# Kernel optimization log

Measured on AMD Instinct MI355X. Metric: run time of the kernel, lower is better.

The kernel has to match this reference:

```python
import jax, jax.numpy as jnp
import numpy as np
from jax import lax

FEAT = 256      # feat_channels
GROUPS = 32     # GN num_groups
NCLS = 80       # num_classes - 1
NRAYS = 36      # polar mask rays
STACK = 4       # stacked_convs
SIZES = [(160, 256), (80, 128), (40, 64), (20, 32), (10, 16)]
B = 1


def conv(x, w, b=None):
    # 3x3 conv, stride 1, pad 1 (SAME). x: [N,C,H,W], w: [O,I,3,3]
    y = lax.conv_general_dilated(x, w, (1, 1), 'SAME',
                                 dimension_numbers=('NCHW', 'OIHW', 'NCHW'))
    if b is not None:
        y = y + b[None, :, None, None]
    return y


def group_norm(x, g, b, eps=1e-5):
    N, C, H, W = x.shape
    xr = x.reshape(N, GROUPS, C // GROUPS, H, W)
    m = xr.mean(axis=(2, 3, 4), keepdims=True)
    v = xr.var(axis=(2, 3, 4), keepdims=True)
    xr = (xr - m) * jax.lax.rsqrt(v + eps)
    return xr.reshape(N, C, H, W) * g[None, :, None, None] + b[None, :, None, None]


def tower(x, ws, gs, bs):
    # ConvModule: conv (no bias, norm present) -> GN -> ReLU, repeated STACK times
    for i in range(STACK):
        x = jax.nn.relu(group_norm(conv(x, ws[i]), gs[i], bs[i]))
    return x


def setup_inputs() -> dict:
    key = jax.random.key(0)
    ks = jax.random.split(key, 32)
    d = {}
    for l, (h, w) in enumerate(SIZES):
        d[f'feat{l}'] = jax.random.normal(ks[l], (B, FEAT, h, w), dtype=jnp.float32)
    std = 0.01
    for j, name in enumerate(['cls', 'reg', 'msk']):
        d[f'{name}_w'] = jax.random.normal(ks[5 + j], (STACK, FEAT, FEAT, 3, 3), jnp.float32) * std
        d[f'{name}_g'] = jnp.ones((STACK, FEAT), jnp.float32)
        d[f'{name}_b'] = jnp.zeros((STACK, FEAT), jnp.float32)
    bias_cls = float(-np.log((1 - 0.01) / 0.01))  # bias_init_with_prob(0.01)
    d['pcls_w'] = jax.random.normal(ks[10], (NCLS, FEAT, 3, 3), jnp.float32) * std
    d['pcls_b'] = jnp.full((NCLS,), bias_cls, jnp.float32)
    d['preg_w'] = jax.random.normal(ks[11], (4, FEAT, 3, 3), jnp.float32) * std
    d['preg_b'] = jnp.zeros((4,), jnp.float32)
    d['pmsk_w'] = jax.random.normal(ks[12], (NRAYS, FEAT, 3, 3), jnp.float32) * std
    d['pmsk_b'] = jnp.zeros((NRAYS,), jnp.float32)
    d['pctr_w'] = jax.random.normal(ks[13], (1, FEAT, 3, 3), jnp.float32) * std
    d['pctr_b'] = jnp.zeros((1,), jnp.float32)
    d['scales_bbox'] = jnp.ones((5,), jnp.float32)
    d['scales_mask'] = jnp.ones((5,), jnp.float32)
    return d


def reference(feat0, feat1, feat2, feat3, feat4,
              cls_w, cls_g, cls_b, reg_w, reg_g, reg_b, msk_w, msk_g, msk_b,
              pcls_w, pcls_b, preg_w, preg_b, pmsk_w, pmsk_b, pctr_w, pctr_b,
              scales_bbox, scales_mask):
    feats = [feat0, feat1, feat2, feat3, feat4]
    cls_outs, bbox_outs, ctr_outs, mask_outs = [], [], [], []
    for l, x in enumerate(feats):
        cf = tower(x, cls_w, cls_g, cls_b)
        cls_outs.append(conv(cf, pcls_w, pcls_b))
        ctr_outs.append(conv(cf, pctr_w, pctr_b))
        rf = tower(x, reg_w, reg_g, reg_b)
        bbox_outs.append(jnp.exp(conv(rf, preg_w, preg_b) * scales_bbox[l]))
        mf = tower(x, msk_w, msk_g, msk_b)
        mask_outs.append(jnp.exp(conv(mf, pmsk_w, pmsk_b) * scales_mask[l]))
    # multi_apply grouping: (cls_scores, bbox_preds, centernesses, mask_preds)
    return tuple(cls_outs) + tuple(bbox_outs) + tuple(ctr_outs) + tuple(mask_outs)
```

## Files before the change

### kernel.cpp

```cpp
#include <hip/hip_runtime.h>

typedef unsigned short u16;
typedef unsigned int u32;
typedef short bf16x8 __attribute__((ext_vector_type(8)));
typedef float f32x4 __attribute__((ext_vector_type(4)));

__device__ __forceinline__ float bf2f(u16 u) {
  u32 x = ((u32)u) << 16;
  float f;
  __builtin_memcpy(&f, &x, 4);
  return f;
}
__device__ __forceinline__ u16 f2bf(float f) {
  u32 x;
  __builtin_memcpy(&x, &f, 4);
  u32 r = x + 0x7FFFu + ((x >> 16) & 1u);
  return (u16)(r >> 16);
}
__device__ __forceinline__ u32 pack2(float f0, float f1) {
  u32 a, b;
  __builtin_memcpy(&a, &f0, 4);
  __builtin_memcpy(&b, &f1, 4);
  a += 0x8000u;
  b += 0x8000u;
  return __builtin_amdgcn_perm(b, a, 0x07060302);
}
__device__ __forceinline__ void glds16(const u16* g, u16* l) {
  __builtin_amdgcn_global_load_lds((const __attribute__((address_space(1))) u32*)g,
                                   (__attribute__((address_space(3))) u32*)l, 16, 0, 0);
}


__global__ void convert_weights(const float* __restrict__ cw, const float* __restrict__ rw,
                                const float* __restrict__ mw, const float* __restrict__ pc,
                                const float* __restrict__ pr, const float* __restrict__ pm,
                                const float* __restrict__ pt, u16* __restrict__ dst) {
  int e = blockIdx.x * 256 + threadIdx.x;
  if (e >= 7446528) return;
  float v = 0.f;
  if (e < 7077888) {
    int conv = e / 589824, r = e % 589824;
    int mo = r / 294912;
    int r2 = r - mo * 294912;
    int kt = r2 >> 12;
    int r3 = r2 & 4095;
    int wm = r3 >> 11;
    int mi = (r3 >> 9) & 3;
    int l = (r3 >> 3) & 63;
    int j = r3 & 7;
    int ch = kt / 9, ti = kt - ch * 9;
    int dxs = ti / 3, dys = ti - dxs * 3;
    int tap = dys * 3 + dxs;
    int o = mo * 128 + wm * 64 + mi * 16 + (l & 15);
    int c = ch * 32 + (l >> 4) * 8 + j;
    const float* s = (conv < 4) ? cw : (conv < 8) ? rw : mw;
    int si = conv & 3;
    v = s[((si * 256 + o) * 256 + c) * 9 + tap];
  } else {
    int e2 = e - 7077888;
    if (e2 < 221184) {
      int chunk = e2 / 27648, r = e2 % 27648;
      int tap = r / 3072, r2 = r % 3072;
      int g = r2 / 768;
      int o = (r2 - g * 768) >> 3;
      int c = chunk * 32 + g * 8 + (r2 & 7);
      if (o < 80) v = pc[(o * 256 + c) * 9 + tap];
      else if (o == 80) v = pt[c * 9 + tap];
    } else if (e2 < 258048) {
      int e3 = e2 - 221184;
      int chunk = e3 / 4608, r = e3 % 4608;
      int tap = r / 512, r2 = r % 512;
      int g = r2 >> 7;
      int o = (r2 >> 3) & 15;
      int c = chunk * 32 + g * 8 + (r2 & 7);
      if (o < 4) v = pr[(o * 256 + c) * 9 + tap];
    } else {
      int e3 = e2 - 258048;
      int chunk = e3 / 13824, r = e3 % 13824;
      int tap = r / 1536, r2 = r % 1536;
      int g = r2 / 384;
      int o = (r2 - g * 384) >> 3;
      int c = chunk * 32 + g * 8 + (r2 & 7);
      if (o < 36) v = pm[(o * 256 + c) * 9 + tap];
    }
  }
  dst[e] = f2bf(v);
}

__global__ void halo_zero(u16* __restrict__ X, u16* __restrict__ Y, long ACT, int ntw) {
  int i = blockIdx.x * 256 + threadIdx.x;
  int rep = i / 26112;
  int j = i - rep * 26112;
  if (rep >= 2 * ntw) return;
  int hp = j >> 4, sub = j & 15;
  int Wp, Hp, pxb, h;
  if (hp < 836)       { Wp = 258; Hp = 162; pxb = 0;     h = hp; }
  else if (hp < 1256) { Wp = 130; Hp = 82;  pxb = 41796; h = hp - 836; }
  else if (hp < 1468) { Wp = 66;  Hp = 42;  pxb = 52456; h = hp - 1256; }
  else if (hp < 1576) { Wp = 34;  Hp = 22;  pxb = 55228; h = hp - 1468; }
  else                { Wp = 18;  Hp = 12;  pxb = 55976; h = hp - 1576; }
  int y, x;
  if (h < Wp)          { y = 0;      x = h; }
  else if (h < 2 * Wp) { y = Hp - 1; x = h - Wp; }
  else {
    int rr = h - 2 * Wp;
    y = 1 + (rr >> 1);
    x = (rr & 1) ? (Wp - 1) : 0;
  }
  u16* buf = (rep < ntw) ? (X + rep * ACT) : (Y + (rep - ntw) * ACT);
  long adr = (long)(pxb + y * Wp + x) * 256 + sub * 16;
  uint4 z = {0, 0, 0, 0};
  *(uint4*)(buf + adr) = z;
  *(uint4*)(buf + adr + 8) = z;
}

__global__ void feat_to_nhwc(const float* __restrict__ f0, const float* __restrict__ f1,
                             const float* __restrict__ f2, const float* __restrict__ f3,
                             const float* __restrict__ f4, u16* __restrict__ dst,
                             long tstride, int nrep) {
  __shared__ float lds[64 * 65];
  int bx = blockIdx.x;
  int tile = bx >> 2, c0 = (bx & 3) * 64;
  int tl, sh, pxb, npx;
  const float* src;
  if (tile < 640)      { tl = tile;       sh = 8; pxb = 0;     npx = 40960; src = f0; }
  else if (tile < 800) { tl = tile - 640; sh = 7; pxb = 41796; npx = 10240; src = f1; }
  else if (tile < 840) { tl = tile - 800; sh = 6; pxb = 52456; npx = 2560;  src = f2; }
  else if (tile < 850) { tl = tile - 840; sh = 5; pxb = 55228; npx = 640;   src = f3; }
  else                 { tl = tile - 850; sh = 4; pxb = 55976; npx = 160;   src = f4; }
  int W = 1 << sh, Wp = W + 2;
  int px0 = tl * 64;
  int t = threadIdx.x;
  {
    int cc = (t >> 6) * 16, px = t & 63;
    bool ok = (px0 + px) < npx;
#pragma unroll
    for (int j = 0; j < 16; ++j) {
      float v = ok ? src[(c0 + cc + j) * npx + px0 + px] : 0.f;
      lds[(cc + j) * 65 + px] = v;
    }
  }
  __syncthreads();
  {
    int px = t >> 2, cL = (t & 3) * 16;
    int pxi = px0 + px;
    if (pxi < npx) {
      int y = pxi >> sh, x = pxi & (W - 1);
      u32 w[8];
#pragma unroll
      for (int j = 0; j < 8; ++j)
        w[j] = pack2(lds[(cL + 2 * j) * 65 + px], lds[(cL + 2 * j + 1) * 65 + px]);
      long adr = (long)(pxb + (y + 1) * Wp + (x + 1)) * 256 + c0 + cL;
      uint4 v0 = {w[0], w[1], w[2], w[3]}, v1 = {w[4], w[5], w[6], w[7]};
      for (int r = 0; r < nrep; ++r) {
        *(uint4*)(dst + r * tstride + adr) = v0;
        *(uint4*)(dst + r * tstride + adr + 8) = v1;
      }
    }
  }
}

__global__ void finalize_stats(const float* __restrict__ stats, int st_ts,
                               const float* __restrict__ g0, const float* __restrict__ g1,
                               const float* __restrict__ g2, const float* __restrict__ b0,
                               const float* __restrict__ b1, const float* __restrict__ b2,
                               float* __restrict__ scaleb, int sb_ts, int ntw) {
  int i = blockIdx.x * 256 + threadIdx.x;
  if (i >= ntw * 1280) return;
  int tw = i / 1280, r = i - tw * 1280, lvl = r >> 8, c = r & 255, g = c >> 3;
  float cnt = (lvl == 0) ? 327680.f : (lvl == 1) ? 81920.f
              : (lvl == 2) ? 20480.f : (lvl == 3) ? 5120.f : 1280.f;
  float s1 = stats[tw * st_ts + (lvl * 32 + g) * 2];
  float s2 = stats[tw * st_ts + (lvl * 32 + g) * 2 + 1];
  float mean = s1 / cnt;
  float var = s2 / cnt - mean * mean;
  float inv = rsqrtf(fmaxf(var, 0.f) + 1e-5f);
  const float* ga = (tw == 0) ? g0 : (tw == 1) ? g1 : g2;
  const float* be = (tw == 0) ? b0 : (tw == 1) ? b1 : b2;
  float sc = inv * ga[c];
  scaleb[(long)tw * sb_ts + (lvl * 256 + c) * 2] = sc;
  scaleb[(long)tw * sb_ts + (lvl * 256 + c) * 2 + 1] = be[c] - mean * sc;
}

__global__ __launch_bounds__(256, 3) void conv_tower(
    const u16* __restrict__ Xn, long in_ts, const u16* __restrict__ Wt, long wt_ts,
    u16* __restrict__ Yraw, long out_ts, float* __restrict__ stats, int st_ts,
    const float* __restrict__ scaleb, int sb_ts, int do_gn) {
  __shared__ __align__(16) u16 Btile[5760];
  __shared__ float shSB[512];
  __shared__ float sred[32];
  int bx = blockIdx.x;
  int tw = bx / 856, r856 = bx - tw * 856;
  Xn += tw * in_ts; Wt += tw * wt_ts; Yraw += tw * out_ts; stats += tw * st_ts;
  int tile = r856 >> 1, mo = r856 & 1;
  int tloc, W, H, SX, pxb, lvl;
  if (tile < 320)      { lvl = 0; tloc = tile;       W = 256; H = 160; SX = 4; pxb = 0; }
  else if (tile < 400) { lvl = 1; tloc = tile - 320; W = 128; H = 80;  SX = 3; pxb = 41796; }
  else if (tile < 420) { lvl = 2; tloc = tile - 400; W = 64;  H = 40;  SX = 2; pxb = 52456; }
  else if (tile < 426) { lvl = 3; tloc = tile - 420; W = 32;  H = 20;  SX = 1; pxb = 55228; }
  else                 { lvl = 4; tloc = tile - 426; W = 16;  H = 10;  SX = 0; pxb = 55976; }
  int Wp = W + 2;
  int ty = tloc >> SX, txi = tloc & ((1 << SX) - 1);
  int y0 = ty * 8, x0 = txi * 16;
  int t = threadIdx.x, lane = t & 63, wave = t >> 6;
  int wm = wave >> 1, wn = wave & 1;
  int quad = lane >> 4, col = lane & 15;
  const u16* Xbase = Xn + (long)(pxb + y0 * Wp + x0) * 256;
  const u16* Wb = Wt + (long)mo * 294912 + wm * 2048 + (long)lane * 8;
  int bcol = quad * 1440 + wn * 576 + col * 8;
  if (do_gn) {
    float2 sv = *(const float2*)(scaleb + (long)tw * sb_ts + (lvl * 256 + t) * 2);
    *(float2*)(&shSB[t * 2]) = sv;
  }
  const u16* Pptr[3];
  int Lo[3], Cb[3];
  bool Uok[3], Keep[3];
#pragma unroll
  for (int i = 0; i < 3; ++i) {
    int u = t + i * 256;
    Uok[i] = u < 720;
    int q = u & 3, p = u >> 2;
    int py = p / 18, px = p - py * 18;
    Pptr[i] = Xbase + (long)(py * Wp + px) * 256 + q * 8;
    Lo[i] = q * 1440 + p * 8;
    Cb[i] = q * 8;
    int yg = y0 + py, xg = x0 + px;
    Keep[i] = (yg >= 1) && (yg <= H) && (xg >= 1) && (xg <= W);
  }
  uint4 breg[3];
#pragma unroll
  for (int i = 0; i < 3; ++i)
    if (Uok[i]) breg[i] = *(const uint4*)(Pptr[i]);
  bf16x8 areg[2][4];
#pragma unroll
  for (int mi = 0; mi < 4; ++mi) areg[0][mi] = *(const bf16x8*)(Wb + mi * 512);
  f32x4 acc[4][4] = {};
  for (int ch = 0; ch < 8; ++ch) {
    __syncthreads();
#pragma unroll
    for (int i = 0; i < 3; ++i) {
      if (Uok[i]) {
        uint4 v = breg[i];
        if (do_gn) {
          int cb2 = (Cb[i] + ch * 32) * 2;
          float4 s01 = *(const float4*)(&shSB[cb2]);
          float4 s23 = *(const float4*)(&shSB[cb2 + 4]);
          float4 s45 = *(const float4*)(&shSB[cb2 + 8]);
          float4 s67 = *(const float4*)(&shSB[cb2 + 12]);
          u32 wv[4] = {v.x, v.y, v.z, v.w};
          float sc[8] = {s01.x, s01.z, s23.x, s23.z, s45.x, s45.z, s67.x, s67.z};
          float bi[8] = {s01.y, s01.w, s23.y, s23.w, s45.y, s45.w, s67.y, s67.w};
          bool kp = Keep[i];
          u32 ow[4];
#pragma unroll
          for (int jj = 0; jj < 4; ++jj) {
            float f0 = bf2f((u16)(wv[jj] & 0xffff)) * sc[2 * jj] + bi[2 * jj];
            float f1 = bf2f((u16)(wv[jj] >> 16)) * sc[2 * jj + 1] + bi[2 * jj + 1];
            f0 = kp ? fmaxf(f0, 0.f) : 0.f;
            f1 = kp ? fmaxf(f1, 0.f) : 0.f;
            ow[jj] = pack2(f0, f1);
          }
          v.x = ow[0]; v.y = ow[1]; v.z = ow[2]; v.w = ow[3];
        }
        *(uint4*)(Btile + Lo[i]) = v;
      }
    }
    __syncthreads();
    if (ch < 7) {
#pragma unroll
      for (int i = 0; i < 3; ++i)
        if (Uok[i]) breg[i] = *(const uint4*)(Pptr[i] + (ch + 1) * 32);
    }
    bf16x8 brow[6];
#pragma unroll
    for (int ti = 0; ti < 9; ++ti) {
      int kt = ch * 9 + ti;
      int dxq = ti / 3, dyq = ti - dxq * 3;
      if (dyq == 0) {
#pragma unroll
        for (int r = 0; r < 6; ++r)
          brow[r] = *(const bf16x8*)(Btile + bcol + r * 144 + dxq * 8);
      }
      if (kt < 71) {
        const u16* wn_ = Wb + (long)(kt + 1) * 4096;
#pragma unroll
        for (int mi = 0; mi < 4; ++mi)
          areg[(ti + 1) & 1][mi] = *(const bf16x8*)(wn_ + mi * 512);
      }
#pragma unroll
      for (int ni = 0; ni < 4; ++ni) {
        bf16x8 b = brow[dyq + ni];
#pragma unroll
        for (int mi = 0; mi < 4; ++mi)
          acc[mi][ni] =
              __builtin_amdgcn_mfma_f32_16x16x32_bf16(areg[ti & 1][mi], b, acc[mi][ni], 0, 0, 0);
      }
    }
#pragma unroll
    for (int mi = 0; mi < 4; ++mi) areg[0][mi] = areg[1][mi];
  }
  if (t < 32) sred[t] = 0.f;
  __syncthreads();
  long pebase = (long)(pxb + (y0 + 1) * Wp + (x0 + col + 1)) * 256;
#pragma unroll
  for (int ni = 0; ni < 4; ++ni) {
    int row = wn * 4 + ni;
    if (y0 + row < H) {
#pragma unroll
      for (int mi = 0; mi < 4; ++mi) {
        f32x4 v = acc[mi][ni];
        int o = mo * 128 + wm * 64 + mi * 16 + quad * 4;
        uint2 pk;
        pk.x = pack2(v[0], v[1]);
        pk.y = pack2(v[2], v[3]);
        *(uint2*)(Yraw + pebase + (long)row * Wp * 256 + o) = pk;
      }
    }
  }
#pragma unroll
  for (int mi = 0; mi < 4; ++mi) {
    float s1 = 0.f, s2 = 0.f;
#pragma unroll
    for (int ni = 0; ni < 4; ++ni) {
      if (y0 + wn * 4 + ni < H) {
        f32x4 v = acc[mi][ni];
#pragma unroll
        for (int r2 = 0; r2 < 4; ++r2) { float f = v[r2]; s1 += f; s2 += f * f; }
      }
    }
#pragma unroll
    for (int m = 1; m < 16; m <<= 1) { s1 += __shfl_xor(s1, m); s2 += __shfl_xor(s2, m); }
    if (col == 0) {
      int g = (wm * 64 + mi * 16 + quad * 4) >> 3;
      atomicAdd(&sred[g * 2], s1);
      atomicAdd(&sred[g * 2 + 1], s2);
    }
  }
  __syncthreads();
  if (t < 32) atomicAdd(&stats[(lvl * 32 + mo * 16 + (t >> 1)) * 2 + (t & 1)], sred[t]);
}

__global__ void gn_relu(u16* __restrict__ buf, long tstride,
                        const float* __restrict__ scaleb, int sb_ts) {
  int i = blockIdx.x * 256 + threadIdx.x;
  int tw = i / 1745920;
  int j = i - tw * 1745920;
  buf += tw * tstride;
  const float* sbp = scaleb + (long)tw * sb_ts;
  int px = j >> 5, cg = j & 31, c0 = cg << 3;
  int lvl, sh, pxb, rem;
  if (px < 40960)      { lvl = 0; rem = px;         sh = 8; pxb = 0;     }
  else if (px < 51200) { lvl = 1; rem = px - 40960; sh = 7; pxb = 41796; }
  else if (px < 53760) { lvl = 2; rem = px - 51200; sh = 6; pxb = 52456; }
  else if (px < 54400) { lvl = 3; rem = px - 53760; sh = 5; pxb = 55228; }
  else                 { lvl = 4; rem = px - 54400; sh = 4; pxb = 55976; }
  int W = 1 << sh;
  int y = rem >> sh, x = rem & (W - 1);
  long adr = (long)(pxb + (y + 1) * (W + 2) + (x + 1)) * 256 + c0;
  uint4 rv = *(const uint4*)(buf + adr);
  const float* pc = sbp + (lvl * 256 + c0) * 2;
  float4 q0 = *(const float4*)(pc);
  float4 q1 = *(const float4*)(pc + 4);
  float4 q2 = *(const float4*)(pc + 8);
  float4 q3 = *(const float4*)(pc + 12);
  float sc[8] = {q0.x, q0.z, q1.x, q1.z, q2.x, q2.z, q3.x, q3.z};
  float bi[8] = {q0.y, q0.w, q1.y, q1.w, q2.y, q2.w, q3.y, q3.w};
  u32 w[4] = {rv.x, rv.y, rv.z, rv.w};
  u32 ow[4];
#pragma unroll
  for (int jj = 0; jj < 4; ++jj) {
    float v0 = fmaxf(bf2f((u16)(w[jj] & 0xffff)) * sc[2 * jj] + bi[2 * jj], 0.f);
    float v1 = fmaxf(bf2f((u16)(w[jj] >> 16)) * sc[2 * jj + 1] + bi[2 * jj + 1], 0.f);
    ow[jj] = pack2(v0, v1);
  }
  uint4 sv = {ow[0], ow[1], ow[2], ow[3]};
  *(uint4*)(buf + adr) = sv;
}

__global__ __launch_bounds__(256, 2) void conv_head_fused(
    const u16* __restrict__ Xbase, long ACT, int htsel, const u16* __restrict__ Whead,
    float* __restrict__ out, const float* __restrict__ pcb, const float* __restrict__ ptb,
    const float* __restrict__ prb, const float* __restrict__ pmb,
    const float* __restrict__ sb, const float* __restrict__ sm) {
  __shared__ u16 Alds[3072];
  __shared__ u16 Blds[2048];
  int bx = blockIdx.x;
  int ht, r;
  if (htsel >= 0) { ht = htsel; r = bx; }
  else { ht = bx / 853; r = bx - ht * 853; }
  int mt, woff;
  const float* bias0;
  const float* scl;
  if (ht == 0)      { mt = 96; woff = 0;      bias0 = pcb; scl = sb; }
  else if (ht == 1) { mt = 16; woff = 221184; bias0 = prb; scl = sb; }
  else              { mt = 48; woff = 258048; bias0 = pmb; scl = sm; }
  const u16* Xn = Xbase + ((htsel >= 0) ? 0 : (long)ht * ACT);
  const u16* Wh = Whead + woff;
  int mt32 = mt * 32, MI = mt >> 4;
  int lvl, tloc, W, H, SX, pxb, npx;
  if (r < 640)      { lvl = 0; tloc = r;       W = 256; H = 160; SX = 4; pxb = 0;     npx = 40960; }
  else if (r < 800) { lvl = 1; tloc = r - 640; W = 128; H = 80;  SX = 3; pxb = 41796; npx = 10240; }
  else if (r < 840) { lvl = 2; tloc = r - 800; W = 64;  H = 40;  SX = 2; pxb = 52456; npx = 2560;  }
  else if (r < 850) { lvl = 3; tloc = r - 840; W = 32;  H = 20;  SX = 1; pxb = 55228; npx = 640;   }
  else              { lvl = 4; tloc = r - 850; W = 16;  H = 10;  SX = 0; pxb = 55976; npx = 160;   }
  int obm, obc = 0;
  if (ht == 0) {
    const int obms[5] = {0, 3276800, 4096000, 4300800, 4352000};
    const int obcs[5] = {4583040, 4624000, 4634240, 4636800, 4637440};
    obm = obms[lvl]; obc = obcs[lvl];
  } else if (ht == 1) {
    const int obms[5] = {4364800, 4528640, 4569600, 4579840, 4582400};
    obm = obms[lvl];
  } else {
    const int obms[5] = {4637600, 6112160, 6480800, 6572960, 6596000};
    obm = obms[lvl];
  }
  int Wp = W + 2;
  int ty = tloc >> SX, txi = tloc & ((1 << SX) - 1);
  int y0 = ty * 4, x0 = txi * 16;
  int t = threadIdx.x, lane = t & 63, wave = t >> 6;
  int quad = lane >> 4, col = lane & 15;
  bool edge = (y0 + 5 > H + 1);
  int rr = (t & 63) >> 4, cc = t & 15, gg = t >> 6;
  const u16* Xrow = Xn + (long)(pxb + (y0 + rr) * Wp + (x0 + cc)) * 256 + gg * 8;
  int aoff = quad * (mt * 8) + col * 8;
  int boff = quad * 512 + (wave * 16 + col) * 8;
  f32x4 acc[6] = {};
  for (int ch = 0; ch < 8; ++ch) {
#pragma unroll
    for (int tap = 0; tap < 9; ++tap) {
      int dy = tap / 3, dx = tap - dy * 3;
      const u16* ws = Wh + (ch * 9 + tap) * mt32;
      int ta = t * 8;
      if (ta < mt32) glds16(ws + ta, Alds + ta);
      int tb = ta + 2048;
      if (tb < mt32) glds16(ws + tb, Alds + tb);
      const u16* xsrc = Xrow + ch * 32 + (dy * Wp + dx) * 256;
      if (!edge) {
        glds16(xsrc, Blds + t * 8);
      } else {
        int yp = y0 + rr + dy;
        uint4 v = {0, 0, 0, 0};
        if (yp <= H + 1) v = *(const uint4*)xsrc;
        *(uint4*)(Blds + t * 8) = v;
      }
      __syncthreads();
      bf16x8 b = *(const bf16x8*)(Blds + boff);
#pragma unroll
      for (int mi = 0; mi < 6; ++mi) {
        if (mi < MI) {
          bf16x8 a = *(const bf16x8*)(Alds + aoff + mi * 128);
          acc[mi] = __builtin_amdgcn_mfma_f32_16x16x32_bf16(a, b, acc[mi], 0, 0, 0);
        }
      }
      __syncthreads();
    }
  }
  int y = y0 + wave;
  if (y < H) {
    float sc = scl[lvl];
    int x = x0 + col;
#pragma unroll
    for (int mi = 0; mi < 6; ++mi) {
      if (mi < MI) {
#pragma unroll
        for (int r2 = 0; r2 < 4; ++r2) {
          int o = mi * 16 + quad * 4 + r2;
          float v = acc[mi][r2];
          if (ht == 0) {
            if (o < 80) out[obm + o * npx + y * W + x] = v + bias0[o];
            else if (o == 80) out[obc + y * W + x] = v + ptb[0];
          } else if (ht == 1) {
            if (o < 4) out[obm + o * npx + y * W + x] = expf((v + bias0[o]) * sc);
          } else {
            if (o < 36) out[obm + o * npx + y * W + x] = expf((v + bias0[o]) * sc);
          }
        }
      }
    }
  }
}

extern "C" void kernel_launch(void* const* d_in, const int* in_sizes, int n_in,
                              void* d_out, int out_size, void* d_ws, size_t ws_size,
                              hipStream_t stream) {
  const float* feat0 = (const float*)d_in[0];
  const float* feat1 = (const float*)d_in[1];
  const float* feat2 = (const float*)d_in[2];
  const float* feat3 = (const float*)d_in[3];
  const float* feat4 = (const float*)d_in[4];
  const float* cw = (const float*)d_in[5];
  const float* rw = (const float*)d_in[8];
  const float* mw = (const float*)d_in[11];
  const float* gmas[3] = {(const float*)d_in[6], (const float*)d_in[9], (const float*)d_in[12]};
  const float* btas[3] = {(const float*)d_in[7], (const float*)d_in[10], (const float*)d_in[13]};
  const float* pcw = (const float*)d_in[14];
  const float* pcb = (const float*)d_in[15];
  const float* prw = (const float*)d_in[16];
  const float* prb = (const float*)d_in[17];
  const float* pmw = (const float*)d_in[18];
  const float* pmb = (const float*)d_in[19];
  const float* ptw = (const float*)d_in[20];
  const float* ptb = (const float*)d_in[21];
  const float* sb = (const float*)d_in[22];
  const float* sm = (const float*)d_in[23];
  float* out = (float*)d_out;

  const long ACT = 14385152;
  const long ACTB = 28770304;
  const long WTS = 14893056;
  char* base = (char*)d_ws;
  u16* wts = (u16*)base;

  size_t need_fused = WTS + 6 * (size_t)ACTB + 3840 + 30720 + 65536;

  convert_weights<<<29088, 256, 0, stream>>>(cw, rw, mw, pcw, prw, pmw, ptw, wts);

  if (ws_size >= need_fused) {
    u16* X = (u16*)(base + WTS);
    u16* Y = (u16*)(base + WTS + 3 * ACTB);
    float* stats = (float*)(base + WTS + 6 * ACTB);
    float* scaleb = (float*)(base + WTS + 6 * ACTB + 3840);
    halo_zero<<<612, 256, 0, stream>>>(X, Y, ACT, 3);
    feat_to_nhwc<<<3412, 256, 0, stream>>>(feat0, feat1, feat2, feat3, feat4, X, ACT, 1);
    for (int s = 0; s < 4; ++s) {
      u16* in = (s & 1) ? Y : X;
      u16* ot = (s & 1) ? X : Y;
      long ints = (s == 0) ? 0 : ACT;
      hipMemsetAsync(stats, 0, 3840, stream);
      conv_tower<<<2568, 256, 0, stream>>>(in, ints, wts + s * 589824, 4 * 589824, ot, ACT,
                                           stats, 320, scaleb, 2560, s > 0);
      finalize_stats<<<15, 256, 0, stream>>>(stats, 320,
                                             gmas[0] + s * 256, gmas[1] + s * 256, gmas[2] + s * 256,
                                             btas[0] + s * 256, btas[1] + s * 256, btas[2] + s * 256,
                                             scaleb, 2560, 3);
    }
    gn_relu<<<20460, 256, 0, stream>>>(X, ACT, scaleb, 2560);
    conv_head_fused<<<2559, 256, 0, stream>>>(X, ACT, -1, wts + 7077888, out,
                                              pcb, ptb, prb, pmb, sb, sm);
  } else {
    u16* bufA = (u16*)(base + WTS);
    u16* bufB = (u16*)(base + WTS + ACTB);
    float* stats = (float*)(base + WTS + 2 * ACTB);
    float* scaleb = (float*)(base + WTS + 2 * ACTB + 1280);
    halo_zero<<<204, 256, 0, stream>>>(bufA, bufB, 0, 1);
    for (int tw = 0; tw < 3; ++tw) {
      feat_to_nhwc<<<3412, 256, 0, stream>>>(feat0, feat1, feat2, feat3, feat4, bufA, 0, 1);
      for (int s = 0; s < 4; ++s) {
        u16* in = (s & 1) ? bufB : bufA;
        u16* ot = (s & 1) ? bufA : bufB;
        hipMemsetAsync(stats, 0, 1280, stream);
        conv_tower<<<856, 256, 0, stream>>>(in, 0, wts + (tw * 4 + s) * 589824, 0, ot, 0,
                                            stats, 0, scaleb, 0, s > 0);
        finalize_stats<<<5, 256, 0, stream>>>(stats, 0,
                                              gmas[tw] + s * 256, gmas[tw] + s * 256, gmas[tw] + s * 256,
                                              btas[tw] + s * 256, btas[tw] + s * 256, btas[tw] + s * 256,
                                              scaleb, 0, 1);
      }
      gn_relu<<<6820, 256, 0, stream>>>(bufA, 0, scaleb, 0);
      conv_head_fused<<<853, 256, 0, stream>>>(bufA, 0, tw, wts + 7077888, out,
                                               pcb, ptb, prb, pmb, sb, sm);
    }
  }
}
```

Before: 1.081 ms.

## Fuse final GN+ReLU into head conv and retile head with register-resident weights

Removes the separate gn_relu pass by applying the last tower's GroupNorm scale/bias, ReLU, and halo zeroing while staging input tiles into LDS inside the head convolution. The head kernel now uses the same halo-tile scheme as the tower conv: an 8x16 pixel tile per block with weights streamed directly into registers and double-buffered, instead of per-tap LDS staging with two syncs per tap. Weight conversion for the head is reordered to match the new per-lane register layout. The weight prefetch guard is dropped, so the final iteration reads one chunk past the end of each head weight block.

```diff
diff --git a/kernel.cpp b/kernel.cpp
--- a/kernel.cpp
+++ b/kernel.cpp
@@ -24,10 +24,6 @@
   a += 0x8000u;
   b += 0x8000u;
   return __builtin_amdgcn_perm(b, a, 0x07060302);
-}
-__device__ __forceinline__ void glds16(const u16* g, u16* l) {
-  __builtin_amdgcn_global_load_lds((const __attribute__((address_space(1))) u32*)g,
-                                   (__attribute__((address_space(3))) u32*)l, 16, 0, 0);
 }
 
 
@@ -58,31 +54,31 @@
     v = s[((si * 256 + o) * 256 + c) * 9 + tap];
   } else {
     int e2 = e - 7077888;
+    int kt, r2, mi, mtsel;
+    const float* src = nullptr;
+    int olim = 0;
+    bool ctr = false;
     if (e2 < 221184) {
-      int chunk = e2 / 27648, r = e2 % 27648;
-      int tap = r / 3072, r2 = r % 3072;
-      int g = r2 / 768;
-      int o = (r2 - g * 768) >> 3;
-      int c = chunk * 32 + g * 8 + (r2 & 7);
-      if (o < 80) v = pc[(o * 256 + c) * 9 + tap];
-      else if (o == 80) v = pt[c * 9 + tap];
+      kt = e2 / 3072; r2 = e2 % 3072; mi = r2 / 512; r2 %= 512;
+      src = pc; olim = 80; ctr = true;
     } else if (e2 < 258048) {
       int e3 = e2 - 221184;
-      int chunk = e3 / 4608, r = e3 % 4608;
-      int tap = r / 512, r2 = r % 512;
-      int g = r2 >> 7;
-      int o = (r2 >> 3) & 15;
-      int c = chunk * 32 + g * 8 + (r2 & 7);
-      if (o < 4) v = pr[(o * 256 + c) * 9 + tap];
+      kt = e3 / 512; r2 = e3 % 512; mi = 0;
+      src = pr; olim = 4;
     } else {
       int e3 = e2 - 258048;
-      int chunk = e3 / 13824, r = e3 % 13824;
-      int tap = r / 1536, r2 = r % 1536;
-      int g = r2 / 384;
-      int o = (r2 - g * 384) >> 3;
-      int c = chunk * 32 + g * 8 + (r2 & 7);
-      if (o < 36) v = pm[(o * 256 + c) * 9 + tap];
-    }
+      kt = e3 / 1536; r2 = e3 % 1536; mi = r2 / 512; r2 %= 512;
+      src = pm; olim = 36;
+    }
+    int l = r2 >> 3, j = r2 & 7;
+    int ch = kt / 9, ti = kt - ch * 9;
+    int dxs = ti / 3, dys = ti - dxs * 3;
+    int tap = dys * 3 + dxs;
+    int o = mi * 16 + (l & 15);
+    int c = ch * 32 + (l >> 4) * 8 + j;
+    if (o < olim) v = src[(o * 256 + c) * 9 + tap];
+    else if (ctr && o == 80) v = pt[c * 9 + tap];
+    (void)mtsel;
   }
   dst[e] = f2bf(v);
 }
@@ -281,7 +277,7 @@
         for (int r = 0; r < 6; ++r)
           brow[r] = *(const bf16x8*)(Btile + bcol + r * 144 + dxq * 8);
       }
-      if (kt < 71) {
+      {
         const u16* wn_ = Wb + (long)(kt + 1) * 4096;
 #pragma unroll
         for (int mi = 0; mi < 4; ++mi)
@@ -340,69 +336,31 @@
   if (t < 32) atomicAdd(&stats[(lvl * 32 + mo * 16 + (t >> 1)) * 2 + (t & 1)], sred[t]);
 }
 
-__global__ void gn_relu(u16* __restrict__ buf, long tstride,
-                        const float* __restrict__ scaleb, int sb_ts) {
-  int i = blockIdx.x * 256 + threadIdx.x;
-  int tw = i / 1745920;
-  int j = i - tw * 1745920;
-  buf += tw * tstride;
-  const float* sbp = scaleb + (long)tw * sb_ts;
-  int px = j >> 5, cg = j & 31, c0 = cg << 3;
-  int lvl, sh, pxb, rem;
-  if (px < 40960)      { lvl = 0; rem = px;         sh = 8; pxb = 0;     }
-  else if (px < 51200) { lvl = 1; rem = px - 40960; sh = 7; pxb = 41796; }
-  else if (px < 53760) { lvl = 2; rem = px - 51200; sh = 6; pxb = 52456; }
-  else if (px < 54400) { lvl = 3; rem = px - 53760; sh = 5; pxb = 55228; }
-  else                 { lvl = 4; rem = px - 54400; sh = 4; pxb = 55976; }
-  int W = 1 << sh;
-  int y = rem >> sh, x = rem & (W - 1);
-  long adr = (long)(pxb + (y + 1) * (W + 2) + (x + 1)) * 256 + c0;
-  uint4 rv = *(const uint4*)(buf + adr);
-  const float* pc = sbp + (lvl * 256 + c0) * 2;
-  float4 q0 = *(const float4*)(pc);
-  float4 q1 = *(const float4*)(pc + 4);
-  float4 q2 = *(const float4*)(pc + 8);
-  float4 q3 = *(const float4*)(pc + 12);
-  float sc[8] = {q0.x, q0.z, q1.x, q1.z, q2.x, q2.z, q3.x, q3.z};
-  float bi[8] = {q0.y, q0.w, q1.y, q1.w, q2.y, q2.w, q3.y, q3.w};
-  u32 w[4] = {rv.x, rv.y, rv.z, rv.w};
-  u32 ow[4];
-#pragma unroll
-  for (int jj = 0; jj < 4; ++jj) {
-    float v0 = fmaxf(bf2f((u16)(w[jj] & 0xffff)) * sc[2 * jj] + bi[2 * jj], 0.f);
-    float v1 = fmaxf(bf2f((u16)(w[jj] >> 16)) * sc[2 * jj + 1] + bi[2 * jj + 1], 0.f);
-    ow[jj] = pack2(v0, v1);
-  }
-  uint4 sv = {ow[0], ow[1], ow[2], ow[3]};
-  *(uint4*)(buf + adr) = sv;
-}
-
-__global__ __launch_bounds__(256, 2) void conv_head_fused(
+__global__ __launch_bounds__(256, 3) void conv_head_fused(
     const u16* __restrict__ Xbase, long ACT, int htsel, const u16* __restrict__ Whead,
     float* __restrict__ out, const float* __restrict__ pcb, const float* __restrict__ ptb,
     const float* __restrict__ prb, const float* __restrict__ pmb,
-    const float* __restrict__ sb, const float* __restrict__ sm) {
-  __shared__ u16 Alds[3072];
-  __shared__ u16 Blds[2048];
+    const float* __restrict__ sb, const float* __restrict__ sm,
+    const float* __restrict__ scaleb, long sb_ts) {
+  __shared__ __align__(16) u16 Btile[5760];
+  __shared__ float shSB[512];
   int bx = blockIdx.x;
   int ht, r;
   if (htsel >= 0) { ht = htsel; r = bx; }
-  else { ht = bx / 853; r = bx - ht * 853; }
-  int mt, woff;
+  else { ht = bx / 428; r = bx - ht * 428; }
+  int MI, woff, mt32;
   const float* bias0;
   const float* scl;
-  if (ht == 0)      { mt = 96; woff = 0;      bias0 = pcb; scl = sb; }
-  else if (ht == 1) { mt = 16; woff = 221184; bias0 = prb; scl = sb; }
-  else              { mt = 48; woff = 258048; bias0 = pmb; scl = sm; }
+  if (ht == 0)      { MI = 6; woff = 0;      mt32 = 3072; bias0 = pcb; scl = sb; }
+  else if (ht == 1) { MI = 1; woff = 221184; mt32 = 512;  bias0 = prb; scl = sb; }
+  else              { MI = 3; woff = 258048; mt32 = 1536; bias0 = pmb; scl = sm; }
   const u16* Xn = Xbase + ((htsel >= 0) ? 0 : (long)ht * ACT);
-  const u16* Wh = Whead + woff;
-  int mt32 = mt * 32, MI = mt >> 4;
-  int lvl, tloc, W, H, SX, pxb, npx;
-  if (r < 640)      { lvl = 0; tloc = r;       W = 256; H = 160; SX = 4; pxb = 0;     npx = 40960; }
-  else if (r < 800) { lvl = 1; tloc = r - 640; W = 128; H = 80;  SX = 3; pxb = 41796; npx = 10240; }
-  else if (r < 840) { lvl = 2; tloc = r - 800; W = 64;  H = 40;  SX = 2; pxb = 52456; npx = 2560;  }
-  else if (r < 850) { lvl = 3; tloc = r - 840; W = 32;  H = 20;  SX = 1; pxb = 55228; npx = 640;   }
-  else              { lvl = 4; tloc = r - 850; W = 16;  H = 10;  SX = 0; pxb = 55976; npx = 160;   }
+  int tloc, W, H, SX, pxb, lvl, npx;
+  if (r < 320)      { lvl = 0; tloc = r;       W = 256; H = 160; SX = 4; pxb = 0;     npx = 40960; }
+  else if (r < 400) { lvl = 1; tloc = r - 320; W = 128; H = 80;  SX = 3; pxb = 41796; npx = 10240; }
+  else if (r < 420) { lvl = 2; tloc = r - 400; W = 64;  H = 40;  SX = 2; pxb = 52456; npx = 2560;  }
+  else if (r < 426) { lvl = 3; tloc = r - 420; W = 32;  H = 20;  SX = 1; pxb = 55228; npx = 640;   }
+  else              { lvl = 4; tloc = r - 426; W = 16;  H = 10;  SX = 0; pxb = 55976; npx = 160;   }
   int obm, obc = 0;
   if (ht == 0) {
     const int obms[5] = {0, 3276800, 4096000, 4300800, 4352000};
@@ -417,63 +375,125 @@
   }
   int Wp = W + 2;
   int ty = tloc >> SX, txi = tloc & ((1 << SX) - 1);
-  int y0 = ty * 4, x0 = txi * 16;
+  int y0 = ty * 8, x0 = txi * 16;
   int t = threadIdx.x, lane = t & 63, wave = t >> 6;
   int quad = lane >> 4, col = lane & 15;
-  bool edge = (y0 + 5 > H + 1);
-  int rr = (t & 63) >> 4, cc = t & 15, gg = t >> 6;
-  const u16* Xrow = Xn + (long)(pxb + (y0 + rr) * Wp + (x0 + cc)) * 256 + gg * 8;
-  int aoff = quad * (mt * 8) + col * 8;
-  int boff = quad * 512 + (wave * 16 + col) * 8;
-  f32x4 acc[6] = {};
+  const u16* Xb2 = Xn + (long)(pxb + y0 * Wp + x0) * 256;
+  const u16* Wb = Whead + woff + (long)lane * 8;
+  {
+    float2 sv = *(const float2*)(scaleb + ht * sb_ts + (lvl * 256 + t) * 2);
+    *(float2*)(&shSB[t * 2]) = sv;
+  }
+  const u16* Pptr[3];
+  int Lo[3], Cb[3];
+  bool Uok[3], Keep[3];
+#pragma unroll
+  for (int i = 0; i < 3; ++i) {
+    int u = t + i * 256;
+    Uok[i] = u < 720;
+    int q = u & 3, p = u >> 2;
+    int py = p / 18, px = p - py * 18;
+    Pptr[i] = Xb2 + (long)(py * Wp + px) * 256 + q * 8;
+    Lo[i] = q * 1440 + p * 8;
+    Cb[i] = q * 8;
+    int yg = y0 + py, xg = x0 + px;
+    Keep[i] = (yg >= 1) && (yg <= H) && (xg >= 1) && (xg <= W);
+  }
+  uint4 breg[3];
+#pragma unroll
+  for (int i = 0; i < 3; ++i)
+    if (Uok[i]) breg[i] = *(const uint4*)(Pptr[i]);
+  bf16x8 areg[2][6];
+#pragma unroll
+  for (int mi = 0; mi < 6; ++mi)
+    if (mi < MI) areg[0][mi] = *(const bf16x8*)(Wb + mi * 512);
+  f32x4 acc[6][2] = {};
+  int brbase = quad * 1440 + wave * 288 + col * 8;
   for (int ch = 0; ch < 8; ++ch) {
-#pragma unroll
-    for (int tap = 0; tap < 9; ++tap) {
-      int dy = tap / 3, dx = tap - dy * 3;
-      const u16* ws = Wh + (ch * 9 + tap) * mt32;
-      int ta = t * 8;
-      if (ta < mt32) glds16(ws + ta, Alds + ta);
-      int tb = ta + 2048;
-      if (tb < mt32) glds16(ws + tb, Alds + tb);
-      const u16* xsrc = Xrow + ch * 32 + (dy * Wp + dx) * 256;
-      if (!edge) {
-        glds16(xsrc, Blds + t * 8);
-      } else {
-        int yp = y0 + rr + dy;
-        uint4 v = {0, 0, 0, 0};
-        if (yp <= H + 1) v = *(const uint4*)xsrc;
-        *(uint4*)(Blds + t * 8) = v;
-      }
-      __syncthreads();
-      bf16x8 b = *(const bf16x8*)(Blds + boff);
+    __syncthreads();
+#pragma unroll
+    for (int i = 0; i < 3; ++i) {
+      if (Uok[i]) {
+        uint4 v = breg[i];
+        int cb2 = (Cb[i] + ch * 32) * 2;
+        float4 s01 = *(const float4*)(&shSB[cb2]);
+        float4 s23 = *(const float4*)(&shSB[cb2 + 4]);
+        float4 s45 = *(const float4*)(&shSB[cb2 + 8]);
+        float4 s67 = *(const float4*)(&shSB[cb2 + 12]);
+        u32 wv[4] = {v.x, v.y, v.z, v.w};
+        float sc[8] = {s01.x, s01.z, s23.x, s23.z, s45.x, s45.z, s67.x, s67.z};
+        float bi[8] = {s01.y, s01.w, s23.y, s23.w, s45.y, s45.w, s67.y, s67.w};
+        bool kp = Keep[i];
+        u32 ow[4];
+#pragma unroll
+        for (int jj = 0; jj < 4; ++jj) {
+          float f0 = bf2f((u16)(wv[jj] & 0xffff)) * sc[2 * jj] + bi[2 * jj];
+          float f1 = bf2f((u16)(wv[jj] >> 16)) * sc[2 * jj + 1] + bi[2 * jj + 1];
+          f0 = kp ? fmaxf(f0, 0.f) : 0.f;
+          f1 = kp ? fmaxf(f1, 0.f) : 0.f;
+          ow[jj] = pack2(f0, f1);
+        }
+        v.x = ow[0]; v.y = ow[1]; v.z = ow[2]; v.w = ow[3];
+        *(uint4*)(Btile + Lo[i]) = v;
+      }
+    }
+    __syncthreads();
+    if (ch < 7) {
+#pragma unroll
+      for (int i = 0; i < 3; ++i)
+        if (Uok[i]) breg[i] = *(const uint4*)(Pptr[i] + (ch + 1) * 32);
+    }
+    bf16x8 brow[4];
+#pragma unroll
+    for (int ti = 0; ti < 9; ++ti) {
+      int kt = ch * 9 + ti;
+      int dxq = ti / 3, dyq = ti - dxq * 3;
+      if (dyq == 0) {
+#pragma unroll
+        for (int rr = 0; rr < 4; ++rr)
+          brow[rr] = *(const bf16x8*)(Btile + brbase + rr * 144 + dxq * 8);
+      }
+      {
+        const u16* wn_ = Wb + (long)(kt + 1) * mt32;
+#pragma unroll
+        for (int mi = 0; mi < 6; ++mi)
+          if (mi < MI) areg[(ti + 1) & 1][mi] = *(const bf16x8*)(wn_ + mi * 512);
+      }
+#pragma unroll
+      for (int ni = 0; ni < 2; ++ni) {
+        bf16x8 b = brow[dyq + ni];
+#pragma unroll
+        for (int mi = 0; mi < 6; ++mi)
+          if (mi < MI)
+            acc[mi][ni] =
+                __builtin_amdgcn_mfma_f32_16x16x32_bf16(areg[ti & 1][mi], b, acc[mi][ni], 0, 0, 0);
+      }
+    }
+#pragma unroll
+    for (int mi = 0; mi < 6; ++mi)
+      if (mi < MI) areg[0][mi] = areg[1][mi];
+  }
+  float scv = scl[lvl];
+  int x = x0 + col;
+#pragma unroll
+  for (int ni = 0; ni < 2; ++ni) {
+    int y = y0 + 2 * wave + ni;
+    if (y < H) {
 #pragma unroll
       for (int mi = 0; mi < 6; ++mi) {
         if (mi < MI) {
-          bf16x8 a = *(const bf16x8*)(Alds + aoff + mi * 128);
-          acc[mi] = __builtin_amdgcn_mfma_f32_16x16x32_bf16(a, b, acc[mi], 0, 0, 0);
-        }
-      }
-      __syncthreads();
-    }
-  }
-  int y = y0 + wave;
-  if (y < H) {
-    float sc = scl[lvl];
-    int x = x0 + col;
-#pragma unroll
-    for (int mi = 0; mi < 6; ++mi) {
-      if (mi < MI) {
-#pragma unroll
-        for (int r2 = 0; r2 < 4; ++r2) {
-          int o = mi * 16 + quad * 4 + r2;
-          float v = acc[mi][r2];
-          if (ht == 0) {
-            if (o < 80) out[obm + o * npx + y * W + x] = v + bias0[o];
-            else if (o == 80) out[obc + y * W + x] = v + ptb[0];
-          } else if (ht == 1) {
-            if (o < 4) out[obm + o * npx + y * W + x] = expf((v + bias0[o]) * sc);
-          } else {
-            if (o < 36) out[obm + o * npx + y * W + x] = expf((v + bias0[o]) * sc);
+#pragma unroll
+          for (int r2 = 0; r2 < 4; ++r2) {
+            int o = mi * 16 + quad * 4 + r2;
+            float v = acc[mi][ni][r2];
+            if (ht == 0) {
+              if (o < 80) out[obm + o * npx + y * W + x] = v + bias0[o];
+              else if (o == 80) out[obc + y * W + x] = v + ptb[0];
+            } else if (ht == 1) {
+              if (o < 4) out[obm + o * npx + y * W + x] = expf((v + bias0[o]) * scv);
+            } else {
+              if (o < 36) out[obm + o * npx + y * W + x] = expf((v + bias0[o]) * scv);
+            }
           }
         }
       }
@@ -535,9 +555,8 @@
                                              btas[0] + s * 256, btas[1] + s * 256, btas[2] + s * 256,
                                              scaleb, 2560, 3);
     }
-    gn_relu<<<20460, 256, 0, stream>>>(X, ACT, scaleb, 2560);
-    conv_head_fused<<<2559, 256, 0, stream>>>(X, ACT, -1, wts + 7077888, out,
-                                              pcb, ptb, prb, pmb, sb, sm);
+    conv_head_fused<<<1284, 256, 0, stream>>>(X, ACT, -1, wts + 7077888, out,
+                                              pcb, ptb, prb, pmb, sb, sm, scaleb, 2560);
   } else {
     u16* bufA = (u16*)(base + WTS);
     u16* bufB = (u16*)(base + WTS + ACTB);
@@ -557,9 +576,8 @@
                                               btas[tw] + s * 256, btas[tw] + s * 256, btas[tw] + s * 256,
                                               scaleb, 0, 1);
       }
-      gn_relu<<<6820, 256, 0, stream>>>(bufA, 0, scaleb, 0);
-      conv_head_fused<<<853, 256, 0, stream>>>(bufA, 0, tw, wts + 7077888, out,
-                                               pcb, ptb, prb, pmb, sb, sm);
-    }
-  }
-}
+      conv_head_fused<<<428, 256, 0, stream>>>(bufA, 0, tw, wts + 7077888, out,
+                                               pcb, ptb, prb, pmb, sb, sm, scaleb, 0);
+    }
+  }
+}
```

Result: faster. 1.003 ms (-7.2%).
